# Kernel optimization log

Measured on AMD Instinct MI355X. Metric: run time of the kernel, lower is better.

## Reference

```python
import jax, jax.numpy as jnp
import numpy as np

N_WIRES = 4
N_LAYERS = 2
BSZ = 4096


def _gate(p):
    # combined single-qubit gate RX(p2) @ RZ(p1) @ RY(p0)  (RY applied first)
    a, b, c = p[0] * 0.5, p[1] * 0.5, p[2] * 0.5
    ca, sa = jnp.cos(a), jnp.sin(a)
    ry = jnp.stack([jnp.stack([ca, -sa]), jnp.stack([sa, ca])]).astype(jnp.complex64)
    eb = (jnp.cos(b) - 1j * jnp.sin(b)).astype(jnp.complex64)  # e^{-i b}
    zero = jnp.zeros((), jnp.complex64)
    rz = jnp.stack([jnp.stack([eb, zero]), jnp.stack([zero, jnp.conj(eb)])])
    cc, sc = jnp.cos(c), jnp.sin(c)
    rx = jnp.stack([jnp.stack([cc + 0j, -1j * sc]), jnp.stack([-1j * sc, cc + 0j])]).astype(jnp.complex64)
    return rx @ rz @ ry


def _apply1(state, U, w):
    # state: (N,2,2,2,2); apply 2x2 gate U on wire w
    s = jnp.moveaxis(state, w + 1, 4)
    s = jnp.einsum('nijka,ba->nijkb', s, U)
    return jnp.moveaxis(s, 4, w + 1)


def _cnot(state, c, t):
    s = jnp.moveaxis(state, (c + 1, t + 1), (1, 2))
    s = jnp.stack([s[:, 0], jnp.flip(s[:, 1], axis=1)], axis=1)
    return jnp.moveaxis(s, (1, 2), (c + 1, t + 1))


def _quanv(x, params):
    bsz = x.shape[0]
    # extract 2x2 patches in the same order as the torch loop:
    # [x[r,c], x[r,c+1], x[r+1,c], x[r+1,c+1]], row-major over (r,c)
    p = x.reshape(bsz, 14, 2, 14, 2).transpose(0, 1, 3, 2, 4).reshape(bsz * 196, 4)
    h = p * 0.5
    v = jnp.stack([jnp.cos(h), jnp.sin(h)], axis=-1).astype(jnp.complex64)  # (N,4,2): RY(patch)|0>
    state = jnp.einsum('na,nb,nc,nd->nabcd', v[:, 0], v[:, 1], v[:, 2], v[:, 3])
    for l in range(N_LAYERS):
        for w in range(N_WIRES):
            state = _apply1(state, _gate(params[l, w]), w)
        for w in range(N_WIRES - 1):
            state = _cnot(state, w, w + 1)
        state = _cnot(state, N_WIRES - 1, 0)
    probs = state.real ** 2 + state.imag ** 2  # (N,2,2,2,2)
    z = jnp.array([1.0, -1.0], jnp.float32)
    exps = []
    for w in range(N_WIRES):
        axes = tuple(i for i in range(1, 5) if i != w + 1)
        exps.append(probs.sum(axes) @ z)  # <Z_w>, shape (N,)
    # (N,4) -> (bsz, 196, 4) -> (bsz, 784), patch-major / wire-minor like torch.cat
    return jnp.stack(exps, axis=-1).reshape(bsz, 196 * N_WIRES)


def setup_inputs() -> dict:
    key = jax.random.key(0)
    k1, k2 = jax.random.split(key)
    x = jax.random.uniform(k1, (BSZ, 28, 28), dtype=jnp.float32)
    params = jax.random.normal(k2, (N_LAYERS, N_WIRES, 3), dtype=jnp.float32)
    return {"x": x, "params": params}


def reference(x, params):
    return _quanv(x, params)
```

## Files before the change

kernel.cpp:

```cpp
#include <hip/hip_runtime.h>


typedef float v2f __attribute__((ext_vector_type(2)));

__device__ __forceinline__ v2f pkfma(v2f a, v2f b, v2f c) {
    return __builtin_elementwise_fma(a, b, c);
}
__device__ __forceinline__ v2f pkcmul(v2f a, v2f b) {
    const v2f t = a.yy * b.yx;
    return pkfma(a.xx, b, (v2f){-t.x, t.y});
}
__device__ __forceinline__ void bfly(v2f A, v2f An, v2f B, v2f Bn, v2f& x0, v2f& x1) {
    const v2f x0s = x0.yx, x1s = x1.yx;
    const v2f y0 = pkfma(A, x0, pkfma(An, x0s, pkfma(B, x1, Bn * x1s)));
    const v2f y1 = pkfma(-B, x0, pkfma(Bn, x0s, pkfma(A, x1, (-An) * x1s)));
    x0 = y0; x1 = y1;
}

__global__ __launch_bounds__(256, 4) void quanv_kernel(
        const float* __restrict__ x,
        const float* __restrict__ params,
        float* __restrict__ out)
{
    __shared__ float4 Gs[8];
    __shared__ v2f    G2[8][4];
    const int t = threadIdx.x;
    if (t < 8) {
        const float* p = params + t * 3;
        const float a = 0.5f * p[0], b = 0.5f * p[1], c = 0.5f * p[2];
        const float sa = __sinf(a), ca = __cosf(a);
        const float sb = __sinf(b), cb = __cosf(b);
        const float sc = __sinf(c), cc = __cosf(c);
        const float ax = cc*ca*cb + sc*sa*sb;
        const float ay = -(cc*ca*sb + sc*sa*cb);
        const float bx = sc*ca*sb - cc*sa*cb;
        const float by = cc*sa*sb - sc*ca*cb;
        Gs[t] = make_float4(ax, ay, bx, by);
        G2[t][0] = (v2f){ax, ax};
        G2[t][1] = (v2f){-ay, ay};
        G2[t][2] = (v2f){bx, bx};
        G2[t][3] = (v2f){-by, by};
    }
    __syncthreads();

    const int gid = blockIdx.x * 256 + t;
    const int n = gid / 196;
    const int p = gid - n * 196;
    const int r = p / 14;
    const int c = p - r * 14;

    const float* xb = x + n * 784 + r * 56 + c * 2;
    const float2 top = *(const float2*)(xb);
    const float2 bot = *(const float2*)(xb + 28);

    float pw[4] = {0.5f * top.x, 0.5f * top.y, 0.5f * bot.x, 0.5f * bot.y};
    v2f wv[4][2];
#pragma unroll
    for (int w = 0; w < 4; ++w) {
        const float cw = __cosf(pw[w]);
        const float sw = __sinf(pw[w]);
        const float4 g = Gs[w];
        wv[w][0] = (v2f){fmaf(g.z, sw, g.x * cw),  fmaf(g.w, sw, g.y * cw)};
        wv[w][1] = (v2f){fmaf(g.x, sw, -g.z * cw), fmaf(-g.y, sw, g.w * cw)};
    }

    v2f ab[4], cd[4];
#pragma unroll
    for (int i = 0; i < 2; ++i)
#pragma unroll
        for (int j = 0; j < 2; ++j) {
            ab[i * 2 + j] = pkcmul(wv[0][i], wv[1][j]);
            cd[i * 2 + j] = pkcmul(wv[2][i], wv[3][j]);
        }
    v2f s[16];
#pragma unroll
    for (int hi = 0; hi < 4; ++hi)
#pragma unroll
        for (int lo = 0; lo < 4; ++lo)
            s[hi * 4 + lo] = pkcmul(ab[hi], cd[lo]);

#pragma unroll
    for (int k = 0; k < 4; ++k) {
        const int bc = 8 >> k;
        const int bt = 8 >> ((k + 1) & 3);
#pragma unroll
        for (int i = 0; i < 16; ++i)
            if ((i & bc) && !(i & bt)) { const v2f tmp = s[i]; s[i] = s[i | bt]; s[i | bt] = tmp; }
    }

#pragma unroll
    for (int w = 0; w < 4; ++w) {
        const int g = 4 + w;
        const v2f A = G2[g][0], An = G2[g][1], B = G2[g][2], Bn = G2[g][3];
        const int bit = 8 >> w;
#pragma unroll
        for (int i = 0; i < 16; ++i) {
            if (i & bit) continue;
            bfly(A, An, B, Bn, s[i], s[i | bit]);
        }
    }

#pragma unroll
    for (int k = 0; k < 4; ++k) {
        const int bc = 8 >> k;
        const int bt = 8 >> ((k + 1) & 3);
#pragma unroll
        for (int i = 0; i < 16; ++i)
            if ((i & bc) && !(i & bt)) { const v2f tmp = s[i]; s[i] = s[i | bt]; s[i | bt] = tmp; }
    }

    float pr[16];
#pragma unroll
    for (int i = 0; i < 16; ++i)
        pr[i] = fmaf(s[i].x, s[i].x, s[i].y * s[i].y);

    const float t00 = pr[0] + pr[1] + pr[2]  + pr[3];
    const float t01 = pr[4] + pr[5] + pr[6]  + pr[7];
    const float t10 = pr[8] + pr[9] + pr[10] + pr[11];
    const float t11 = pr[12] + pr[13] + pr[14] + pr[15];
    const float e0 = (t00 + t01) - (t10 + t11);
    const float e1 = (t00 - t01) + (t10 - t11);

    const float u00 = pr[0] + pr[4] + pr[8]  + pr[12];
    const float u01 = pr[1] + pr[5] + pr[9]  + pr[13];
    const float u10 = pr[2] + pr[6] + pr[10] + pr[14];
    const float u11 = pr[3] + pr[7] + pr[11] + pr[15];
    const float e2 = (u00 + u01) - (u10 + u11);
    const float e3 = (u00 - u01) + (u10 - u11);

    *(float4*)(out + gid * 4) = make_float4(e0, e1, e2, e3);
}

extern "C" void kernel_launch(void* const* d_in, const int* in_sizes, int n_in,
                              void* d_out, int out_size, void* d_ws, size_t ws_size,
                              hipStream_t stream) {
    const float* x      = (const float*)d_in[0];
    const float* params = (const float*)d_in[1];
    float* out = (float*)d_out;

    const int npatch = 4096 * 196;
    quanv_kernel<<<npatch / 256, 256, 0, stream>>>(x, params, out);
}
```

Measured before the change: 76.41 us.

## Apply second-layer unitary and CNOT permutations via fp16 MFMA matrix multiply

```diff
diff --git a/kernel.cpp b/kernel.cpp
--- a/kernel.cpp
+++ b/kernel.cpp
@@ -1,21 +1,16 @@
 #include <hip/hip_runtime.h>
 
 
-typedef float v2f __attribute__((ext_vector_type(2)));
+typedef _Float16 f16;
+typedef _Float16 half8 __attribute__((ext_vector_type(8)));
+typedef float f4 __attribute__((ext_vector_type(4)));
 
-__device__ __forceinline__ v2f pkfma(v2f a, v2f b, v2f c) {
-    return __builtin_elementwise_fma(a, b, c);
+__device__ __forceinline__ float2 cmulf(float2 a, float2 b) {
+    return make_float2(fmaf(a.x, b.x, -(a.y * b.y)),
+                       fmaf(a.x, b.y,   a.y * b.x));
 }
-__device__ __forceinline__ v2f pkcmul(v2f a, v2f b) {
-    const v2f t = a.yy * b.yx;
-    return pkfma(a.xx, b, (v2f){-t.x, t.y});
-}
-__device__ __forceinline__ void bfly(v2f A, v2f An, v2f B, v2f Bn, v2f& x0, v2f& x1) {
-    const v2f x0s = x0.yx, x1s = x1.yx;
-    const v2f y0 = pkfma(A, x0, pkfma(An, x0s, pkfma(B, x1, Bn * x1s)));
-    const v2f y1 = pkfma(-B, x0, pkfma(Bn, x0s, pkfma(A, x1, (-An) * x1s)));
-    x0 = y0; x1 = y1;
-}
+
+#define PK2(a, b) __builtin_bit_cast(float, __builtin_amdgcn_cvt_pkrtz((a), (b)))
 
 __global__ __launch_bounds__(256, 4) void quanv_kernel(
         const float* __restrict__ x,
@@ -23,8 +18,11 @@
         float* __restrict__ out)
 {
     __shared__ float4 Gs[8];
-    __shared__ v2f    G2[8][4];
+    __shared__ __align__(16) f16 Wt[32][40];
+    __shared__ __align__(16) unsigned char SB[4][5120];
+
     const int t = threadIdx.x;
+
     if (t < 8) {
         const float* p = params + t * 3;
         const float a = 0.5f * p[0], b = 0.5f * p[1], c = 0.5f * p[2];
@@ -36,12 +34,31 @@
         const float bx = sc*ca*sb - cc*sa*cb;
         const float by = cc*sa*sb - sc*ca*cb;
         Gs[t] = make_float4(ax, ay, bx, by);
-        G2[t][0] = (v2f){ax, ax};
-        G2[t][1] = (v2f){-ay, ay};
-        G2[t][2] = (v2f){bx, bx};
-        G2[t][3] = (v2f){-by, by};
     }
     __syncthreads();
+
+    {
+        const unsigned long long IDX1P = 0x497a2f1c85b6e3d0ULL;
+        const unsigned long long INV1P = 0xa3185ce7d46f2b90ULL;
+        const int i = t >> 4;
+        const int m = t & 15;
+        const int j = (int)((IDX1P >> (i * 4)) & 15);
+        const int k = (int)((INV1P >> (m * 4)) & 15);
+        float2 e = make_float2(1.f, 0.f);
+#pragma unroll
+        for (int w = 0; w < 4; ++w) {
+            const float4 g = Gs[4 + w];
+            const int jb = (j >> (3 - w)) & 1;
+            const int kb = (k >> (3 - w)) & 1;
+            const float ux = jb ? (kb ?  g.x : -g.z) : (kb ? g.z : g.x);
+            const float uy = jb ? (kb ? -g.y :  g.w) : (kb ? g.w : g.y);
+            e = cmulf(e, make_float2(ux, uy));
+        }
+        Wt[i][m]           = (f16)e.x;
+        Wt[i][16 + m]      = (f16)(-e.y);
+        Wt[16 + i][m]      = (f16)e.y;
+        Wt[16 + i][16 + m] = (f16)e.x;
+    }
 
     const int gid = blockIdx.x * 256 + t;
     const int n = gid / 196;
@@ -54,77 +71,88 @@
     const float2 bot = *(const float2*)(xb + 28);
 
     float pw[4] = {0.5f * top.x, 0.5f * top.y, 0.5f * bot.x, 0.5f * bot.y};
-    v2f wv[4][2];
+    float2 wv[4][2];
 #pragma unroll
     for (int w = 0; w < 4; ++w) {
         const float cw = __cosf(pw[w]);
         const float sw = __sinf(pw[w]);
         const float4 g = Gs[w];
-        wv[w][0] = (v2f){fmaf(g.z, sw, g.x * cw),  fmaf(g.w, sw, g.y * cw)};
-        wv[w][1] = (v2f){fmaf(g.x, sw, -g.z * cw), fmaf(-g.y, sw, g.w * cw)};
+        wv[w][0] = make_float2(fmaf(g.z, sw, g.x * cw),  fmaf(g.w, sw, g.y * cw));
+        wv[w][1] = make_float2(fmaf(g.x, sw, -g.z * cw), fmaf(-g.y, sw, g.w * cw));
     }
 
-    v2f ab[4], cd[4];
+    float2 ab[4], cd[4];
 #pragma unroll
     for (int i = 0; i < 2; ++i)
 #pragma unroll
         for (int j = 0; j < 2; ++j) {
-            ab[i * 2 + j] = pkcmul(wv[0][i], wv[1][j]);
-            cd[i * 2 + j] = pkcmul(wv[2][i], wv[3][j]);
+            ab[i * 2 + j] = cmulf(wv[0][i], wv[1][j]);
+            cd[i * 2 + j] = cmulf(wv[2][i], wv[3][j]);
         }
-    v2f s[16];
+    float2 s[16];
 #pragma unroll
     for (int hi = 0; hi < 4; ++hi)
 #pragma unroll
         for (int lo = 0; lo < 4; ++lo)
-            s[hi * 4 + lo] = pkcmul(ab[hi], cd[lo]);
+            s[hi * 4 + lo] = cmulf(ab[hi], cd[lo]);
 
+    const int l   = t & 63;
+    const int wid = t >> 6;
+    const int q   = l >> 4;
+    const int c16 = l & 15;
+
+    f16* st = (f16*)(SB[wid] + l * 80);
+    const float4 r0 = make_float4(PK2(s[0].x, s[1].x),  PK2(s[2].x, s[3].x),
+                                  PK2(s[4].x, s[5].x),  PK2(s[6].x, s[7].x));
+    const float4 r1 = make_float4(PK2(s[8].x, s[9].x),  PK2(s[10].x, s[11].x),
+                                  PK2(s[12].x, s[13].x), PK2(s[14].x, s[15].x));
+    const float4 r2 = make_float4(PK2(s[0].y, s[1].y),  PK2(s[2].y, s[3].y),
+                                  PK2(s[4].y, s[5].y),  PK2(s[6].y, s[7].y));
+    const float4 r3 = make_float4(PK2(s[8].y, s[9].y),  PK2(s[10].y, s[11].y),
+                                  PK2(s[12].y, s[13].y), PK2(s[14].y, s[15].y));
+    *(float4*)(st)      = r0;
+    *(float4*)(st + 8)  = r1;
+    *(float4*)(st + 16) = r2;
+    *(float4*)(st + 24) = r3;
+
+    __syncthreads();
+
+    const half8 b0 = *(const half8*)&Wt[c16][q * 8];
+    const half8 b1 = *(const half8*)&Wt[16 + c16][q * 8];
+    const f4 zf4 = {0.f, 0.f, 0.f, 0.f};
+    f4 d0[4], d1[4];
 #pragma unroll
-    for (int k = 0; k < 4; ++k) {
-        const int bc = 8 >> k;
-        const int bt = 8 >> ((k + 1) & 3);
-#pragma unroll
-        for (int i = 0; i < 16; ++i)
-            if ((i & bc) && !(i & bt)) { const v2f tmp = s[i]; s[i] = s[i | bt]; s[i | bt] = tmp; }
+    for (int m = 0; m < 4; ++m) {
+        const half8 am = *(const half8*)((const f16*)(SB[wid] + (m * 16 + c16) * 80) + q * 8);
+        d0[m] = __builtin_amdgcn_mfma_f32_16x16x32_f16(am, b0, zf4, 0, 0, 0);
+        d1[m] = __builtin_amdgcn_mfma_f32_16x16x32_f16(am, b1, zf4, 0, 0, 0);
     }
 
+    float* prb = (float*)SB[wid];
 #pragma unroll
-    for (int w = 0; w < 4; ++w) {
-        const int g = 4 + w;
-        const v2f A = G2[g][0], An = G2[g][1], B = G2[g][2], Bn = G2[g][3];
-        const int bit = 8 >> w;
+    for (int m = 0; m < 4; ++m)
 #pragma unroll
-        for (int i = 0; i < 16; ++i) {
-            if (i & bit) continue;
-            bfly(A, An, B, Bn, s[i], s[i | bit]);
+        for (int reg = 0; reg < 4; ++reg) {
+            const float pv = fmaf(d0[m][reg], d0[m][reg], d1[m][reg] * d1[m][reg]);
+            prb[(m * 16 + q * 4 + reg) * 20 + c16] = pv;
         }
-    }
 
-#pragma unroll
-    for (int k = 0; k < 4; ++k) {
-        const int bc = 8 >> k;
-        const int bt = 8 >> ((k + 1) & 3);
-#pragma unroll
-        for (int i = 0; i < 16; ++i)
-            if ((i & bc) && !(i & bt)) { const v2f tmp = s[i]; s[i] = s[i | bt]; s[i | bt] = tmp; }
-    }
+    const float4 p0 = *(const float4*)(prb + l * 20);
+    const float4 p1 = *(const float4*)(prb + l * 20 + 4);
+    const float4 p2 = *(const float4*)(prb + l * 20 + 8);
+    const float4 p3 = *(const float4*)(prb + l * 20 + 12);
 
-    float pr[16];
-#pragma unroll
-    for (int i = 0; i < 16; ++i)
-        pr[i] = fmaf(s[i].x, s[i].x, s[i].y * s[i].y);
-
-    const float t00 = pr[0] + pr[1] + pr[2]  + pr[3];
-    const float t01 = pr[4] + pr[5] + pr[6]  + pr[7];
-    const float t10 = pr[8] + pr[9] + pr[10] + pr[11];
-    const float t11 = pr[12] + pr[13] + pr[14] + pr[15];
+    const float t00 = p0.x + p0.y + p0.z + p0.w;
+    const float t01 = p1.x + p1.y + p1.z + p1.w;
+    const float t10 = p2.x + p2.y + p2.z + p2.w;
+    const float t11 = p3.x + p3.y + p3.z + p3.w;
     const float e0 = (t00 + t01) - (t10 + t11);
     const float e1 = (t00 - t01) + (t10 - t11);
 
-    const float u00 = pr[0] + pr[4] + pr[8]  + pr[12];
-    const float u01 = pr[1] + pr[5] + pr[9]  + pr[13];
-    const float u10 = pr[2] + pr[6] + pr[10] + pr[14];
-    const float u11 = pr[3] + pr[7] + pr[11] + pr[15];
+    const float u00 = p0.x + p1.x + p2.x + p3.x;
+    const float u01 = p0.y + p1.y + p2.y + p3.y;
+    const float u10 = p0.z + p1.z + p2.z + p3.z;
+    const float u11 = p0.w + p1.w + p2.w + p3.w;
     const float e2 = (u00 + u01) - (u10 + u11);
     const float e3 = (u00 - u01) + (u10 - u11);
 
```

New measurement: 71.84 us. 6.0% less time.
